# Performance work log

Measured on AMD Instinct MI355X. Metric: run time of the kernel, lower is better.

## Reference

```python
import jax, jax.numpy as jnp
import numpy as np
import math

D_MODEL = 768
NUM_HEADS = 12
D_K = D_MODEL // NUM_HEADS
B, S = 4, 2048


def setup_inputs() -> dict:
    key = jax.random.key(0)
    ks = jax.random.split(key, 11)
    s = 1.0 / math.sqrt(D_MODEL)
    inp = {
        "q": jax.random.normal(ks[0], (B, S, D_MODEL), jnp.float32),
        "k": jax.random.normal(ks[1], (B, S, D_MODEL), jnp.float32),
        "v": jax.random.normal(ks[2], (B, S, D_MODEL), jnp.float32),
        "w_q": jax.random.normal(ks[3], (D_MODEL, D_MODEL), jnp.float32) * s,
        "b_q": jax.random.normal(ks[4], (D_MODEL,), jnp.float32) * s,
        "w_k": jax.random.normal(ks[5], (D_MODEL, D_MODEL), jnp.float32) * s,
        "b_k": jax.random.normal(ks[6], (D_MODEL,), jnp.float32) * s,
        "w_v": jax.random.normal(ks[7], (D_MODEL, D_MODEL), jnp.float32) * s,
        "b_v": jax.random.normal(ks[8], (D_MODEL,), jnp.float32) * s,
        "w_o": jax.random.normal(ks[9], (D_MODEL, D_MODEL), jnp.float32) * s,
        "b_o": jax.random.normal(ks[10], (D_MODEL,), jnp.float32) * s,
    }
    return inp


def reference(q, k, v, w_q, b_q, w_k, b_k, w_v, b_v, w_o, b_o):
    b = q.shape[0]
    # Linear projections (torch Linear: x @ W.T + b), reshape to [B,H,S,d_k]
    def proj(x, w, bias):
        y = x @ w.T + bias
        return y.reshape(b, -1, NUM_HEADS, D_K).transpose(0, 2, 1, 3)

    qh = proj(q, w_q, b_q)
    kh = proj(k, w_k, b_k)
    vh = proj(v, w_v, b_v)

    scale = 1.0 / math.sqrt(D_K)
    scores = jnp.einsum("bhqd,bhkd->bhqk", qh, kh) * scale  # [B,H,S,S]
    attn = jax.nn.softmax(scores, axis=-1)
    # dropout is identity in eval mode
    out = jnp.einsum("bhqk,bhkd->bhqd", attn, vh)
    out = out.transpose(0, 2, 1, 3).reshape(b, -1, D_MODEL)
    return out @ w_o.T + b_o
```

## Files before the change

kernel.cpp:

```cpp
#include <hip/hip_runtime.h>

#define DEV __device__ __forceinline__

typedef __attribute__((ext_vector_type(8))) short short8;
typedef __attribute__((ext_vector_type(4))) float f32x4;
typedef unsigned short u16;
typedef unsigned int u32;

DEV f32x4 mfma16(short8 a, short8 b, f32x4 c) {
    return __builtin_amdgcn_mfma_f32_16x16x32_bf16(a, b, c, 0, 0, 0);
}

DEV u16 f2bf(float f) {
    unsigned u = __builtin_bit_cast(unsigned, f);
    u += 0x7fffu + ((u >> 16) & 1u);
    return (u16)(u >> 16);
}

DEV u32 cvt_pk_bf16(float a, float b) {
    u32 r;
    asm("v_cvt_pk_bf16_f32 %0, %1, %2" : "=v"(r) : "v"(a), "v"(b));
    return r;
}

DEV float fexp2_scaled(float xs) {
    int i = (int)xs + 1065055420;
    return __builtin_bit_cast(float, i);
}

DEV void gload16(const void* g, const void* l) {
    __builtin_amdgcn_global_load_lds(
        (const __attribute__((address_space(1))) unsigned int*)g,
        (__attribute__((address_space(3))) unsigned int*)l, 16, 0, 0);
}

template<int N> DEV void waitvm_barrier() {
    asm volatile("s_waitcnt vmcnt(%0)\n\ts_barrier" :: "n"(N) : "memory");
}

DEV short8 lds_frag_swz(const u16* base, int row, int chunk) {
    int sc = chunk ^ (row & 7);
    return *(const short8*)((const char*)base + row * 128 + sc * 16);
}

__global__ __launch_bounds__(256) void prep(
    const float* __restrict__ q, const float* __restrict__ k, const float* __restrict__ v,
    const float* __restrict__ wq, const float* __restrict__ wk,
    const float* __restrict__ wv, const float* __restrict__ wo,
    u16* __restrict__ xq, u16* __restrict__ xk, u16* __restrict__ xv,
    u16* __restrict__ wqB, u16* __restrict__ wkB, u16* __restrict__ wvB,
    u16* __restrict__ woB)
{
    int b = blockIdx.x;
    const float* s;
    u16* d;
    int i;
    if (b < 18432) {
        int t = b / 6144, r = b % 6144;
        s = t == 0 ? q : t == 1 ? k : v;
        d = t == 0 ? xq : t == 1 ? xk : xv;
        i = r * 256 + threadIdx.x;
    } else {
        int t = (b - 18432) / 576, r = (b - 18432) % 576;
        s = t == 0 ? wq : t == 1 ? wk : t == 2 ? wv : wo;
        d = t == 0 ? wqB : t == 1 ? wkB : t == 2 ? wvB : woB;
        i = r * 256 + threadIdx.x;
    }
    float4 vv = ((const float4*)s)[i];
    ((ushort4*)d)[i] = make_ushort4(f2bf(vv.x), f2bf(vv.y), f2bf(vv.z), f2bf(vv.w));
}

template<int MODE>
DEV void gemm_body(const u16* __restrict__ A_g, const u16* __restrict__ B_g,
                   const float* __restrict__ bias, float scale,
                   u16* __restrict__ outP, float* __restrict__ outF,
                   int mBase, int nBase)
{
    __shared__ u16 AS[64 * 64], BS[128 * 64];

    const int tid = threadIdx.x;
    const int l = tid & 63, wid = tid >> 6;
    const int wy = wid >> 1, wx = wid & 1;
    const int lr = l & 15, lg = l >> 4;

    f32x4 acc[2][4];
    for (int i = 0; i < 2; ++i)
        for (int j = 0; j < 4; ++j) acc[i][j] = (f32x4)0.0f;

    for (int kt = 0; kt < 12; ++kt) {
        if (kt) __syncthreads();
        for (int r = 0; r < 2; ++r) {
            int c = tid + r * 256;
            int row = c >> 3;
            int sc = (c & 7) ^ (row & 7);
            size_t gA = (size_t)(mBase + row) * 768 + kt * 64 + sc * 8;
            gload16(A_g + gA, AS + (size_t)(r * 256 + wid * 64) * 8);
        }
        for (int r = 0; r < 4; ++r) {
            int c = tid + r * 256;
            int row = c >> 3;
            int sc = (c & 7) ^ (row & 7);
            size_t gB = (size_t)(nBase + row) * 768 + kt * 64 + sc * 8;
            gload16(B_g + gB, BS + (size_t)(r * 256 + wid * 64) * 8);
        }
        __syncthreads();

        short8 bf[4][2];
        for (int nt = 0; nt < 4; ++nt)
            for (int ks = 0; ks < 2; ++ks)
                bf[nt][ks] = lds_frag_swz(BS, wx * 64 + nt * 16 + lr, ks * 4 + lg);
        for (int mt = 0; mt < 2; ++mt) {
            short8 ah[2];
            for (int ks = 0; ks < 2; ++ks)
                ah[ks] = lds_frag_swz(AS, wy * 32 + mt * 16 + lr, ks * 4 + lg);
            for (int nt = 0; nt < 4; ++nt)
                for (int ks = 0; ks < 2; ++ks)
                    acc[mt][nt] = mfma16(ah[ks], bf[nt][ks], acc[mt][nt]);
        }
    }

    for (int mt = 0; mt < 2; ++mt)
        for (int nt = 0; nt < 4; ++nt) {
            int colg = nBase + wx * 64 + nt * 16 + lr;
            for (int r = 0; r < 4; ++r) {
                int rowg = mBase + wy * 32 + mt * 16 + lg * 4 + r;
                float bv = (MODE == 2) ? bias[rowg] : bias[colg];
                float vv = (acc[mt][nt][r] + bv) * scale;
                if constexpr (MODE == 0) {
                    int b = rowg >> 11, s = rowg & 2047;
                    int h = colg >> 6, d = colg & 63;
                    outP[((size_t)(b * 12 + h) * 2048 + s) * 64 + d] = f2bf(vv);
                } else if constexpr (MODE == 1) {
                    outF[(size_t)rowg * 768 + colg] = vv;
                } else {
                    int b = colg >> 11, s = colg & 2047;
                    int h = rowg >> 6, d = rowg & 63;
                    outP[((size_t)(b * 12 + h) * 64 + d) * 2048 + s] = f2bf(vv);
                }
            }
        }
}

__global__ __launch_bounds__(256, 4) void gemm_proj(
    const u16* __restrict__ xq, const u16* __restrict__ xk, const u16* __restrict__ xv,
    const u16* __restrict__ wqB, const u16* __restrict__ wkB, const u16* __restrict__ wvB,
    const float* __restrict__ bq, const float* __restrict__ bk, const float* __restrict__ bv,
    u16* __restrict__ Qpl, u16* __restrict__ Kpl, u16* __restrict__ Vtp)
{
    int z = blockIdx.z;
    if (z == 0) {
        gemm_body<0>(xq, wqB, bq, 0.125f * 1.44269504f * 8388608.0f, Qpl, nullptr,
                     blockIdx.y * 64, blockIdx.x * 128);
    } else if (z == 1) {
        gemm_body<0>(xk, wkB, bk, 1.0f, Kpl, nullptr,
                     blockIdx.y * 64, blockIdx.x * 128);
    } else {
        int id = blockIdx.y * 6 + blockIdx.x;
        gemm_body<2>(wvB, xv, bv, 1.0f, Vtp, nullptr,
                     (id % 12) * 64, (id / 12) * 128);
    }
}

__global__ __launch_bounds__(256, 4) void gemm_out(
    const u16* __restrict__ Op, const u16* __restrict__ woB,
    const float* __restrict__ bias, float* __restrict__ outF)
{
    gemm_body<1>(Op, woB, bias, 1.0f, nullptr, outF,
                 blockIdx.y * 64, blockIdx.x * 128);
}

__global__ __launch_bounds__(256, 3) void attn4(
    const u16* __restrict__ Qp, const u16* __restrict__ Kp,
    const u16* __restrict__ Vtp, u16* __restrict__ Op)
{
    __shared__ u16 Ks[2][64 * 64], Vs[2][64 * 64];
    __shared__ u16 Eh[128][72];

    const int tid = threadIdx.x;
    const int l = tid & 63, wid = tid >> 6;
    const int lr = l & 15, lg = l >> 4;
    const int bh = blockIdx.x, qt = blockIdx.y;

    short8 q_h[2][2];
    for (int s = 0; s < 2; ++s) {
        size_t qrow = ((size_t)bh * 2048 + qt * 128 + wid * 32 + s * 16 + lr) * 64;
        q_h[s][0] = *(const short8*)(Qp + qrow + lg * 8);
        q_h[s][1] = *(const short8*)(Qp + qrow + 32 + lg * 8);
    }

    short8 ones;
    for (int j = 0; j < 8; ++j) ones[j] = (short)0x3F80;

    f32x4 num[2][4];
    for (int s = 0; s < 2; ++s)
        for (int nt = 0; nt < 4; ++nt) num[s][nt] = (f32x4)0.0f;
    f32x4 denacc[2] = {(f32x4)0.0f, (f32x4)0.0f};

    auto stageK = [&](int kb, int p) {
        for (int r = 0; r < 2; ++r) {
            int c = tid + r * 256;
            int row = c >> 3, sc = (c & 7) ^ (row & 7);
            size_t g = ((size_t)bh * 2048 + kb * 64 + row) * 64 + sc * 8;
            gload16(Kp + g, Ks[p] + (size_t)(r * 256 + wid * 64) * 8);
        }
    };
    auto stageV = [&](int kb, int p) {
        for (int r = 0; r < 2; ++r) {
            int c = tid + r * 256;
            int row = c >> 3, sc = (c & 7) ^ (row & 7);
            size_t g = ((size_t)bh * 64 + row) * 2048 + kb * 64 + sc * 8;
            gload16(Vtp + g, Vs[p] + (size_t)(r * 256 + wid * 64) * 8);
        }
    };

    stageK(0, 0);
    stageV(0, 0);

    for (int kb = 0; kb < 32; ++kb) {
        const int p = kb & 1;
        waitvm_barrier<0>();
        if (kb < 31) {
            stageK(kb + 1, p ^ 1);
            stageV(kb + 1, p ^ 1);
        }

        f32x4 st[2][4];
        for (int s = 0; s < 2; ++s)
            for (int nt = 0; nt < 4; ++nt) st[s][nt] = (f32x4)0.0f;
        __builtin_amdgcn_s_setprio(1);
        for (int nt = 0; nt < 4; ++nt)
            for (int ks = 0; ks < 2; ++ks) {
                short8 kh = lds_frag_swz(Ks[p], nt * 16 + lr, ks * 4 + lg);
                st[0][nt] = mfma16(kh, q_h[0][ks], st[0][nt]);
                st[1][nt] = mfma16(kh, q_h[1][ks], st[1][nt]);
            }
        __builtin_amdgcn_s_setprio(0);

        for (int s = 0; s < 2; ++s)
            for (int nt = 0; nt < 4; ++nt) {
                u32 pk0 = cvt_pk_bf16(fexp2_scaled(st[s][nt][0]), fexp2_scaled(st[s][nt][1]));
                u32 pk1 = cvt_pk_bf16(fexp2_scaled(st[s][nt][2]), fexp2_scaled(st[s][nt][3]));
                int erow = wid * 32 + s * 16 + lr;
                *(u32*)&Eh[erow][nt * 16 + lg * 4]     = pk0;
                *(u32*)&Eh[erow][nt * 16 + lg * 4 + 2] = pk1;
            }

        short8 e[2][2];
        for (int s = 0; s < 2; ++s) {
            int erow = wid * 32 + s * 16 + lr;
            e[s][0] = *(const short8*)&Eh[erow][lg * 8];
            e[s][1] = *(const short8*)&Eh[erow][32 + lg * 8];
        }
        __builtin_amdgcn_s_setprio(1);
        denacc[0] = mfma16(e[0][0], ones, denacc[0]);
        denacc[0] = mfma16(e[0][1], ones, denacc[0]);
        denacc[1] = mfma16(e[1][0], ones, denacc[1]);
        denacc[1] = mfma16(e[1][1], ones, denacc[1]);
        for (int nt = 0; nt < 4; ++nt)
            for (int ks = 0; ks < 2; ++ks) {
                short8 vh = lds_frag_swz(Vs[p], nt * 16 + lr, ks * 4 + lg);
                num[0][nt] = mfma16(e[0][ks], vh, num[0][nt]);
                num[1][nt] = mfma16(e[1][ks], vh, num[1][nt]);
            }
        __builtin_amdgcn_s_setprio(0);
    }

    const int b = bh / 12, h = bh % 12;
    for (int s = 0; s < 2; ++s) {
        float rden[4];
        for (int r = 0; r < 4; ++r) rden[r] = 1.0f / denacc[s][r];
        for (int nt = 0; nt < 4; ++nt)
            for (int r = 0; r < 4; ++r) {
                int srow = qt * 128 + wid * 32 + s * 16 + lg * 4 + r;
                size_t rowg = (size_t)b * 2048 + srow;
                int col = h * 64 + nt * 16 + lr;
                Op[rowg * 768 + col] = f2bf(num[s][nt][r] * rden[r]);
            }
    }
}

extern "C" void kernel_launch(void* const* d_in, const int* in_sizes, int n_in,
                              void* d_out, int out_size, void* d_ws, size_t ws_size,
                              hipStream_t stream)
{
    const float* q   = (const float*)d_in[0];
    const float* k   = (const float*)d_in[1];
    const float* v   = (const float*)d_in[2];
    const float* w_q = (const float*)d_in[3];
    const float* b_q = (const float*)d_in[4];
    const float* w_k = (const float*)d_in[5];
    const float* b_k = (const float*)d_in[6];
    const float* w_v = (const float*)d_in[7];
    const float* b_v = (const float*)d_in[8];
    const float* w_o = (const float*)d_in[9];
    const float* b_o = (const float*)d_in[10];
    float* out = (float*)d_out;

    const size_t PL  = (size_t)48 * 2048 * 64;
    const size_t WPL = (size_t)768 * 768;
    u16* base = (u16*)d_ws;
    u16* xqB = base;
    u16* xkB = base + PL;
    u16* xvB = base + 2 * PL;
    u16* Qpl = base + 3 * PL;
    u16* Kpl = base + 4 * PL;
    u16* Vtp = base + 5 * PL;
    u16* OP  = base + 6 * PL;
    u16* W   = base + 7 * PL;
    u16* wqB = W;
    u16* wkB = W + WPL;
    u16* wvB = W + 2 * WPL;
    u16* woB = W + 3 * WPL;

    dim3 bt(256, 1, 1);
    hipLaunchKernelGGL(prep, dim3(20736), bt, 0, stream,
                       q, k, v, w_q, w_k, w_v, w_o,
                       xqB, xkB, xvB, wqB, wkB, wvB, woB);

    hipLaunchKernelGGL(gemm_proj, dim3(6, 128, 3), bt, 0, stream,
                       xqB, xkB, xvB, wqB, wkB, wvB, b_q, b_k, b_v,
                       Qpl, Kpl, Vtp);

    hipLaunchKernelGGL(attn4, dim3(48, 16), bt, 0, stream,
                       Qpl, Kpl, Vtp, OP);

    hipLaunchKernelGGL(gemm_out, dim3(6, 128), bt, 0, stream,
                       OP, woB, b_o, out);
}
```

Before: 154.0 us.

## Fuse fp32-to-bf16 activation conversion into projection GEMM tile loads

Removes the separate pass that converted q/k/v activations to bf16. The projection GEMM now reads fp32 activations directly, converts them in registers with v_cvt_pk_bf16 and writes the swizzled bf16 tile to LDS. This cuts a full fp32 read plus bf16 write and re-read of about 75MB of activations. The trade-off is that the async global_load_lds path for that operand becomes synchronous register loads with twice the global bytes per tile. The block index is also remapped into groups of 8 m-tiles per n-column for better L2 reuse.

```diff
diff --git a/kernel.cpp b/kernel.cpp
--- a/kernel.cpp
+++ b/kernel.cpp
@@ -44,34 +44,23 @@
 }
 
 __global__ __launch_bounds__(256) void prep(
-    const float* __restrict__ q, const float* __restrict__ k, const float* __restrict__ v,
     const float* __restrict__ wq, const float* __restrict__ wk,
     const float* __restrict__ wv, const float* __restrict__ wo,
-    u16* __restrict__ xq, u16* __restrict__ xk, u16* __restrict__ xv,
     u16* __restrict__ wqB, u16* __restrict__ wkB, u16* __restrict__ wvB,
     u16* __restrict__ woB)
 {
     int b = blockIdx.x;
-    const float* s;
-    u16* d;
-    int i;
-    if (b < 18432) {
-        int t = b / 6144, r = b % 6144;
-        s = t == 0 ? q : t == 1 ? k : v;
-        d = t == 0 ? xq : t == 1 ? xk : xv;
-        i = r * 256 + threadIdx.x;
-    } else {
-        int t = (b - 18432) / 576, r = (b - 18432) % 576;
-        s = t == 0 ? wq : t == 1 ? wk : t == 2 ? wv : wo;
-        d = t == 0 ? wqB : t == 1 ? wkB : t == 2 ? wvB : woB;
-        i = r * 256 + threadIdx.x;
-    }
+    int t = b / 576, r = b % 576;
+    const float* s = t == 0 ? wq : t == 1 ? wk : t == 2 ? wv : wo;
+    u16* d = t == 0 ? wqB : t == 1 ? wkB : t == 2 ? wvB : woB;
+    int i = r * 256 + threadIdx.x;
     float4 vv = ((const float4*)s)[i];
     ((ushort4*)d)[i] = make_ushort4(f2bf(vv.x), f2bf(vv.y), f2bf(vv.z), f2bf(vv.w));
 }
 
-template<int MODE>
-DEV void gemm_body(const u16* __restrict__ A_g, const u16* __restrict__ B_g,
+template<int AF32, int BF32, int MODE>
+DEV void gemm_body(const float* __restrict__ Af, const u16* __restrict__ A_g,
+                   const float* __restrict__ Bf, const u16* __restrict__ B_g,
                    const float* __restrict__ bias, float scale,
                    u16* __restrict__ outP, float* __restrict__ outF,
                    int mBase, int nBase)
@@ -89,19 +78,43 @@
 
     for (int kt = 0; kt < 12; ++kt) {
         if (kt) __syncthreads();
-        for (int r = 0; r < 2; ++r) {
-            int c = tid + r * 256;
-            int row = c >> 3;
-            int sc = (c & 7) ^ (row & 7);
-            size_t gA = (size_t)(mBase + row) * 768 + kt * 64 + sc * 8;
-            gload16(A_g + gA, AS + (size_t)(r * 256 + wid * 64) * 8);
-        }
-        for (int r = 0; r < 4; ++r) {
-            int c = tid + r * 256;
-            int row = c >> 3;
-            int sc = (c & 7) ^ (row & 7);
-            size_t gB = (size_t)(nBase + row) * 768 + kt * 64 + sc * 8;
-            gload16(B_g + gB, BS + (size_t)(r * 256 + wid * 64) * 8);
+        if constexpr (AF32) {
+            for (int i = 0; i < 4; ++i) {
+                int f = tid + i * 256;
+                int row = f >> 4, q4 = f & 15;
+                float4 xv = *(const float4*)(Af + (size_t)(mBase + row) * 768 + kt * 64 + q4 * 4);
+                u32 lo = cvt_pk_bf16(xv.x, xv.y);
+                u32 hi = cvt_pk_bf16(xv.z, xv.w);
+                int byteOff = row * 128 + (((q4 >> 1) ^ (row & 7)) * 16) + (q4 & 1) * 8;
+                *(uint2*)((char*)AS + byteOff) = make_uint2(lo, hi);
+            }
+        } else {
+            for (int r = 0; r < 2; ++r) {
+                int c = tid + r * 256;
+                int row = c >> 3;
+                int sc = (c & 7) ^ (row & 7);
+                size_t gA = (size_t)(mBase + row) * 768 + kt * 64 + sc * 8;
+                gload16(A_g + gA, AS + (size_t)(r * 256 + wid * 64) * 8);
+            }
+        }
+        if constexpr (BF32) {
+            for (int i = 0; i < 8; ++i) {
+                int f = tid + i * 256;
+                int row = f >> 4, q4 = f & 15;
+                float4 xv = *(const float4*)(Bf + (size_t)(nBase + row) * 768 + kt * 64 + q4 * 4);
+                u32 lo = cvt_pk_bf16(xv.x, xv.y);
+                u32 hi = cvt_pk_bf16(xv.z, xv.w);
+                int byteOff = row * 128 + (((q4 >> 1) ^ (row & 7)) * 16) + (q4 & 1) * 8;
+                *(uint2*)((char*)BS + byteOff) = make_uint2(lo, hi);
+            }
+        } else {
+            for (int r = 0; r < 4; ++r) {
+                int c = tid + r * 256;
+                int row = c >> 3;
+                int sc = (c & 7) ^ (row & 7);
+                size_t gB = (size_t)(nBase + row) * 768 + kt * 64 + sc * 8;
+                gload16(B_g + gB, BS + (size_t)(r * 256 + wid * 64) * 8);
+            }
         }
         __syncthreads();
 
@@ -142,22 +155,29 @@
 }
 
 __global__ __launch_bounds__(256, 4) void gemm_proj(
-    const u16* __restrict__ xq, const u16* __restrict__ xk, const u16* __restrict__ xv,
+    const float* __restrict__ q, const float* __restrict__ k, const float* __restrict__ v,
     const u16* __restrict__ wqB, const u16* __restrict__ wkB, const u16* __restrict__ wvB,
     const float* __restrict__ bq, const float* __restrict__ bk, const float* __restrict__ bv,
     u16* __restrict__ Qpl, u16* __restrict__ Kpl, u16* __restrict__ Vtp)
 {
+    int b = blockIdx.x;
     int z = blockIdx.z;
-    if (z == 0) {
-        gemm_body<0>(xq, wqB, bq, 0.125f * 1.44269504f * 8388608.0f, Qpl, nullptr,
-                     blockIdx.y * 64, blockIdx.x * 128);
-    } else if (z == 1) {
-        gemm_body<0>(xk, wkB, bk, 1.0f, Kpl, nullptr,
-                     blockIdx.y * 64, blockIdx.x * 128);
+    if (z < 2) {
+        int m = (b & 7) + 8 * ((b >> 3) / 6);
+        int n = (b >> 3) % 6;
+        if (z == 0) {
+            gemm_body<1, 0, 0>(q, nullptr, nullptr, wqB, bq,
+                               0.125f * 1.44269504f * 8388608.0f, Qpl, nullptr,
+                               m * 64, n * 128);
+        } else {
+            gemm_body<1, 0, 0>(k, nullptr, nullptr, wkB, bk, 1.0f, Kpl, nullptr,
+                               m * 64, n * 128);
+        }
     } else {
-        int id = blockIdx.y * 6 + blockIdx.x;
-        gemm_body<2>(wvB, xv, bv, 1.0f, Vtp, nullptr,
-                     (id % 12) * 64, (id / 12) * 128);
+        int m = (b >> 3) % 12;
+        int n = (b & 7) + 8 * ((b >> 3) / 12);
+        gemm_body<0, 1, 2>(nullptr, wvB, v, nullptr, bv, 1.0f, Vtp, nullptr,
+                           m * 64, n * 128);
     }
 }
 
@@ -165,8 +185,8 @@
     const u16* __restrict__ Op, const u16* __restrict__ woB,
     const float* __restrict__ bias, float* __restrict__ outF)
 {
-    gemm_body<1>(Op, woB, bias, 1.0f, nullptr, outF,
-                 blockIdx.y * 64, blockIdx.x * 128);
+    gemm_body<0, 0, 1>(nullptr, Op, nullptr, woB, bias, 1.0f, nullptr, outF,
+                       blockIdx.y * 64, blockIdx.x * 128);
 }
 
 __global__ __launch_bounds__(256, 3) void attn4(
@@ -299,26 +319,22 @@
     const size_t PL  = (size_t)48 * 2048 * 64;
     const size_t WPL = (size_t)768 * 768;
     u16* base = (u16*)d_ws;
-    u16* xqB = base;
-    u16* xkB = base + PL;
-    u16* xvB = base + 2 * PL;
-    u16* Qpl = base + 3 * PL;
-    u16* Kpl = base + 4 * PL;
-    u16* Vtp = base + 5 * PL;
-    u16* OP  = base + 6 * PL;
-    u16* W   = base + 7 * PL;
+    u16* Qpl = base;
+    u16* Kpl = base + PL;
+    u16* Vtp = base + 2 * PL;
+    u16* OP  = base + 3 * PL;
+    u16* W   = base + 4 * PL;
     u16* wqB = W;
     u16* wkB = W + WPL;
     u16* wvB = W + 2 * WPL;
     u16* woB = W + 3 * WPL;
 
     dim3 bt(256, 1, 1);
-    hipLaunchKernelGGL(prep, dim3(20736), bt, 0, stream,
-                       q, k, v, w_q, w_k, w_v, w_o,
-                       xqB, xkB, xvB, wqB, wkB, wvB, woB);
-
-    hipLaunchKernelGGL(gemm_proj, dim3(6, 128, 3), bt, 0, stream,
-                       xqB, xkB, xvB, wqB, wkB, wvB, b_q, b_k, b_v,
+    hipLaunchKernelGGL(prep, dim3(2304), bt, 0, stream,
+                       w_q, w_k, w_v, w_o, wqB, wkB, wvB, woB);
+
+    hipLaunchKernelGGL(gemm_proj, dim3(768, 1, 3), bt, 0, stream,
+                       q, k, v, wqB, wkB, wvB, b_q, b_k, b_v,
                        Qpl, Kpl, Vtp);
 
     hipLaunchKernelGGL(attn4, dim3(48, 16), bt, 0, stream,
```

Result: faster. 139.9 us (-9.2%).
